# Performance work log

Hardware: AMD Instinct MI355X
Metric: run time of the kernel (lower is better)

## Reference

```python
import jax, jax.numpy as jnp
import numpy as np


def _lambertw_real(z: float) -> float:
    # real branch W0 for z > e, Newton iteration (static, numpy)
    w = np.log(z) - np.log(np.log(z))
    for _ in range(30):
        ew = np.exp(w)
        w = w - (w * ew - z) / (ew * (w + 1.0))
    return float(w)


def setup_inputs() -> dict:
    key = jax.random.key(0)
    ks = jax.random.split(key, 8)
    B, D, Wd, Hd, heads = 4, 64, 48, 48, 4
    dh = D // heads
    return {
        "x": jax.random.normal(ks[0], (B, D, Wd, Hd), jnp.float32),
        "Wq": jax.random.normal(ks[1], (heads, dh, D), jnp.float32) * 0.05,
        "bq": jax.random.normal(ks[2], (heads, dh), jnp.float32) * 0.05,
        "Wv": jax.random.normal(ks[3], (heads, dh, D), jnp.float32) * 0.05,
        "bv": jax.random.normal(ks[4], (heads, dh), jnp.float32) * 0.05,
        "Wo": jax.random.normal(ks[5], (D, D), jnp.float32) * 0.05,
        "bo": jax.random.normal(ks[6], (D,), jnp.float32) * 0.05,
        "gamma": jax.random.normal(ks[7], (1,), jnp.float32),
    }


def reference(x, Wq, bq, Wv, bv, Wo, bo, gamma):
    B, D, Wd, Hd = x.shape
    heads, dh, _ = Wq.shape
    N = Wd * Hd
    scalar = jnp.sqrt(jnp.asarray(D / heads, jnp.float32))

    x_flat = x.reshape(B, D, N)          # true [B, D, N] layout (1x1 conv input)
    x_r = x.reshape(B, N, D)             # faithful to torch x.view(B, N, D)

    outs = []
    for h in range(heads):
        # q: [B, N, dh] (conv1x1 then permute)
        q = jnp.einsum('kd,bdn->bnk', Wq[h], x_flat) + bq[h][None, None, :]
        qn = jnp.sum(q * q, axis=2)      # squared row norms [B, N]
        # expanded squared L2 distance: ||qi||^2 - 2 qi.qj + ||qj||^2
        dist = qn[:, :, None] - 2.0 * jnp.einsum('bnk,bmk->bnm', q, q) + qn[:, None, :]
        P = jax.nn.softmax(dist / (-scalar), axis=-1)   # [B, N, N]
        # A_h from weight.view(1, D, dh): row-major reshape, NOT transpose
        WqR = Wq[h].reshape(D, dh)
        A = (WqR @ WqR.T) / scalar       # [D, D]
        f = jnp.einsum('bnm,bmd->bnd', P, x_r) @ A      # [B, N, D]
        f_img = f.reshape(B, D, N)       # faithful to .view(B, D, W, H)
        v = jnp.einsum('kd,bdn->bkn', Wv[h], f_img) + bv[h][None, :, None]
        outs.append(v.reshape(B, N, dh))  # faithful to .view(B, N, dh)

    cat = jnp.concatenate(outs, axis=2).reshape(B, D, N)  # .view(B, D, W, H)
    out = jnp.einsum('od,bdn->bon', Wo, cat) + bo[None, :, None]

    # Lipschitz-style bound
    phi = jnp.asarray(_lambertw_real(N / np.e), jnp.float32)
    term = jnp.sqrt(jnp.sum(jnp.sum(Wq * Wq, axis=(1, 2)) * jnp.sum(Wv * Wv, axis=(1, 2))))
    bound = jnp.sqrt(jnp.asarray(N / D, jnp.float32)) * (4.0 * phi + 1.0) * term * jnp.linalg.norm(Wo)

    out = out / bound
    return gamma * out.reshape(B, D, Wd, Hd) + x
```

## Files before the change

kernel.cpp:

```cpp
#include <hip/hip_runtime.h>
#include <math.h>


#define OFF_SC  0
#define OFF_AF  16
#define OFF_QFB 8208
#define OFF_QFA 303120
#define OFF_QN  598032
#define OFF_XF  634896
#define OFF_F2  929808

#define LOG2E 1.44269504f

typedef __attribute__((ext_vector_type(8))) short bf16x8;
typedef __attribute__((ext_vector_type(16))) float f32x16;
union U4 { uint4 u; bf16x8 b; };

__device__ __forceinline__ unsigned short f2bf(float x) {
    unsigned int u = __float_as_uint(x);
    unsigned int r = u + 0x7fffu + ((u >> 16) & 1u);
    return (unsigned short)(r >> 16);
}
__device__ __forceinline__ float bf2f(unsigned short v) {
    return __uint_as_float((unsigned int)v << 16);
}

__global__ __launch_bounds__(256) void k_prep(
    const float* __restrict__ x, const float* __restrict__ Wq,
    const float* __restrict__ bq, const float* __restrict__ Wv,
    const float* __restrict__ Wo, const float* __restrict__ gamma, float* ws)
{
    __shared__ __align__(16) char smem[8192];
    const int bid = blockIdx.x, t = threadIdx.x;

    if (bid == 0) {
        double* red  = (double*)smem;
        double* sums = (double*)(smem + 2048);
        for (int ph = 0; ph < 9; ++ph) {
            double s = 0.0;
            if (ph < 4) {
                const float* W = Wq + ph * 1024;
                for (int i = t; i < 1024; i += 256) { double v = W[i]; s += v * v; }
            } else if (ph < 8) {
                const float* W = Wv + (ph - 4) * 1024;
                for (int i = t; i < 1024; i += 256) { double v = W[i]; s += v * v; }
            } else {
                for (int i = t; i < 4096; i += 256) { double v = Wo[i]; s += v * v; }
            }
            red[t] = s; __syncthreads();
            for (int off = 128; off; off >>= 1) {
                if (t < off) red[t] += red[t + off];
                __syncthreads();
            }
            if (t == 0) sums[ph] = red[0];
            __syncthreads();
        }
        if (t == 0) {
            float z = 2304.0f / 2.7182818284590452f;
            float w = logf(z) - logf(logf(z));
            #pragma unroll 1
            for (int it = 0; it < 30; ++it) {
                float ew = __expf(w);
                w = w - (w * ew - z) / (ew * (w + 1.0f));
            }
            double phi = (double)w;
            double term = sqrt(sums[0]*sums[4] + sums[1]*sums[5] +
                               sums[2]*sums[6] + sums[3]*sums[7]);
            double bound = 6.0 * (4.0 * phi + 1.0) * term * sqrt(sums[8]);
            ws[OFF_SC] = (float)((double)gamma[0] / bound);
        }
    } else if (bid <= 64) {
        float* WlP = (float*)smem;
        int id = bid - 1, h = id >> 4, dq = id & 15;
        const float* W = Wq + h * 1024;
        for (int i = t; i < 1024; i += 256) WlP[(i >> 4) * 17 + (i & 15)] = W[i];
        __syncthreads();
        int dl = t >> 6, e = t & 63, d = dq * 4 + dl;
        float s = 0.f;
        #pragma unroll
        for (int k = 0; k < 16; ++k) s += WlP[d * 17 + k] * WlP[e * 17 + k];
        int tt = d >> 4, j = d & 7, l = ((d >> 3) & 1) * 32 + (e & 31), ec = e >> 5;
        unsigned short* af = (unsigned short*)(ws + OFF_AF);
        af[(((h * 4 + tt) * 2 + ec) * 64 + l) * 8 + j] = f2bf(0.25f * s);
    } else if (bid <= 640) {
        float* WlT = (float*)smem;
        float* bl  = (float*)(smem + 4096);
        float* qnp = (float*)(smem + 4160);
        int rb = bid - 65, bh = rb / 36, nb = rb % 36;
        int h = bh & 3, b = bh >> 2;
        const float* W = Wq + h * 1024;
        for (int i = t; i < 1024; i += 256) WlT[(i & 63) * 16 + (i >> 6)] = W[i];
        if (t < 16) bl[t] = bq[h * 16 + t];
        __syncthreads();
        int nl = t & 63, kg = t >> 6, n = nb * 64 + nl;
        const float* xb = x + (size_t)b * 147456;
        const float4* wrow = (const float4*)WlT;
        float q0 = bl[kg*4], q1 = bl[kg*4+1], q2 = bl[kg*4+2], q3 = bl[kg*4+3];
        for (int d = 0; d < 64; ++d) {
            float xv = xb[d * 2304 + n];
            float4 wv = wrow[d * 4 + kg];
            q0 = fmaf(wv.x, xv, q0); q1 = fmaf(wv.y, xv, q1);
            q2 = fmaf(wv.z, xv, q2); q3 = fmaf(wv.w, xv, q3);
        }
        qnp[kg * 64 + nl] = q0*q0 + q1*q1 + q2*q2 + q3*q3;
        unsigned pB0 = (unsigned)f2bf(q0) | ((unsigned)f2bf(q1) << 16);
        unsigned pB1 = (unsigned)f2bf(q2) | ((unsigned)f2bf(q3) << 16);
        const float sA = 0.5f * LOG2E;
        unsigned pA0 = (unsigned)f2bf(sA*q0) | ((unsigned)f2bf(sA*q1) << 16);
        unsigned pA1 = (unsigned)f2bf(sA*q2) | ((unsigned)f2bf(sA*q3) << 16);
        size_t base = (size_t)(bh * 72 + (n >> 5)) * 256
                    + (size_t)(((kg >> 1) * 32 + (n & 31)) * 4 + (kg & 1) * 2);
        *(uint2*)((unsigned*)((unsigned short*)(ws + OFF_QFB)) + base) = make_uint2(pB0, pB1);
        *(uint2*)((unsigned*)((unsigned short*)(ws + OFF_QFA)) + base) = make_uint2(pA0, pA1);
        __syncthreads();
        if (t < 64) {
            float qn = qnp[t] + qnp[64 + t] + qnp[128 + t] + qnp[192 + t];
            ws[OFF_QN + bh * 2304 + nb * 64 + t] = -0.25f * LOG2E * qn;
        }
    } else {
        int i = (bid - 641) * 256 + t;
        int l = i & 63, c1 = i >> 6;
        int dc = c1 & 1, c2 = c1 >> 1;
        int T = c2 % 144, b = c2 / 144;
        const float* xb = x + (size_t)b * 147456;
        int col = dc * 32 + (l & 31), mbase = 16 * T + (l >> 5) * 8;
        unsigned int pk[4];
        #pragma unroll
        for (int jj = 0; jj < 4; ++jj) {
            float f0 = xb[(mbase + 2*jj) * 64 + col];
            float f1 = xb[(mbase + 2*jj + 1) * 64 + col];
            pk[jj] = (unsigned int)f2bf(f0) | ((unsigned int)f2bf(f1) << 16);
        }
        ((uint4*)((unsigned short*)(ws + OFF_XF)))[i] = make_uint4(pk[0], pk[1], pk[2], pk[3]);
    }
}

__global__ __launch_bounds__(256, 4) void k_attn(float* __restrict__ ws)
{
    __shared__ __align__(16) char smem[40448];
    float* qn_s = (float*)smem;
    float (*Ols)[32][68] = (float (*)[32][68])smem;
    unsigned short (*fls)[80] = (unsigned short (*)[80])(smem + 34816);
    float* Lls = (float*)(smem + 34816 + 5120);

    const int t = threadIdx.x, w = t >> 6, lane = t & 63;
    const int bid = (blockIdx.x & 7) * 144 + (blockIdx.x >> 3);
    const int bh = bid / 72, rc = bid % 72;
    const int h = bh & 3;
    const int b = bh >> 2;
    const int hi = lane >> 5, nl = lane & 31, s4 = hi * 4;

    const uint4* QB = (const uint4*)((const unsigned short*)(ws + OFF_QFB)) + (size_t)bh * 4608;
    const uint4* QA = (const uint4*)((const unsigned short*)(ws + OFF_QFA)) + (size_t)bh * 4608;
    const uint4* XF = (const uint4*)((const unsigned short*)(ws + OFF_XF)) + (size_t)b * 18432;
    const float* qn = ws + OFF_QN + bh * 2304;

    for (int i = t; i < 576; i += 256)
        ((float4*)qn_s)[i] = ((const float4*)qn)[i];

    U4 qb; qb.u = QB[rc * 64 + lane];
    const float qoffl = qn[rc * 32 + nl];

    f32x16 O0, O1;
    #pragma unroll
    for (int i = 0; i < 16; ++i) { O0[i] = 0.f; O1[i] = 0.f; }
    float lrun = 0.f;

    __syncthreads();

    #pragma unroll 2
    for (int it = 0; it < 18; ++it) {
        const int ht = w + it * 4;
        const int m0 = ht * 32;
        U4 xv[4];
        #pragma unroll
        for (int q = 0; q < 4; ++q) xv[q].u = XF[(size_t)(ht * 4 + q) * 64 + lane];
        U4 a0; a0.u = QA[ht * 64 + lane];
        f32x16 c0;
        #pragma unroll
        for (int g = 0; g < 4; ++g) {
            float4 t4 = *(const float4*)(qn_s + m0 + 8 * g + s4);
            c0[4*g+0] = t4.x + qoffl; c0[4*g+1] = t4.y + qoffl;
            c0[4*g+2] = t4.z + qoffl; c0[4*g+3] = t4.w + qoffl;
        }
        f32x16 s0 = __builtin_amdgcn_mfma_f32_32x32x16_bf16(a0.b, qb.b, c0, 0, 0, 0);
        float p[16];
        #pragma unroll
        for (int r = 0; r < 16; ++r)
            asm("v_exp_f32 %0, %1" : "=v"(p[r]) : "v"(s0[r]));
        float la = 0.f, lb = 0.f, lc = 0.f, ld = 0.f;
        #pragma unroll
        for (int r = 0; r < 16; r += 4) {
            la += p[r]; lb += p[r+1]; lc += p[r+2]; ld += p[r+3];
        }
        lrun += (la + lb) + (lc + ld);
        unsigned int wd[8], xd[8];
        #pragma unroll
        for (int i = 0; i < 8; ++i)
            asm("v_cvt_pk_bf16_f32 %0, %1, %2"
                : "=v"(wd[i]) : "v"(p[2*i]), "v"(p[2*i + 1]));
        #pragma unroll
        for (int i = 0; i < 8; ++i) xd[i] = (unsigned int)__shfl_xor((int)wd[i], 32);
        U4 af0, af1;
        af0.u.x = hi ? xd[2] : wd[0];  af0.u.y = hi ? xd[3] : wd[1];
        af0.u.z = hi ? wd[2] : xd[0];  af0.u.w = hi ? wd[3] : xd[1];
        af1.u.x = hi ? xd[6] : wd[4];  af1.u.y = hi ? xd[7] : wd[5];
        af1.u.z = hi ? wd[6] : xd[4];  af1.u.w = hi ? wd[7] : xd[5];
        O0 = __builtin_amdgcn_mfma_f32_32x32x16_bf16(af0.b, xv[0].b, O0, 0, 0, 0);
        O1 = __builtin_amdgcn_mfma_f32_32x32x16_bf16(af0.b, xv[1].b, O1, 0, 0, 0);
        O0 = __builtin_amdgcn_mfma_f32_32x32x16_bf16(af1.b, xv[2].b, O0, 0, 0, 0);
        O1 = __builtin_amdgcn_mfma_f32_32x32x16_bf16(af1.b, xv[3].b, O1, 0, 0, 0);
    }
    __syncthreads();

    lrun += __shfl_xor(lrun, 32);
    #pragma unroll
    for (int r = 0; r < 16; ++r) {
        int n = (r & 3) + 8 * (r >> 2) + s4;
        Ols[w][n][nl]      = O0[r];
        Ols[w][n][nl + 32] = O1[r];
    }
    if (!hi) Lls[w * 32 + nl] = lrun;
    __syncthreads();

    {
        int n = t >> 3, d0 = (t & 7) * 8;
        float invL = 1.f / (Lls[n] + Lls[32 + n] + Lls[64 + n] + Lls[96 + n]);
        float f[8];
        #pragma unroll
        for (int j = 0; j < 8; ++j)
            f[j] = (Ols[0][n][d0+j] + Ols[1][n][d0+j] +
                    Ols[2][n][d0+j] + Ols[3][n][d0+j]) * invL;
        unsigned int pk[4];
        #pragma unroll
        for (int i = 0; i < 4; ++i)
            asm("v_cvt_pk_bf16_f32 %0, %1, %2" : "=v"(pk[i]) : "v"(f[2*i]), "v"(f[2*i+1]));
        *(uint4*)((char*)&fls[0][0] + n * 160 + d0 * 2) = make_uint4(pk[0], pk[1], pk[2], pk[3]);
    }
    __syncthreads();

    if (w < 2) {
        const int ec = w;
        const uint4* AFp = (const uint4*)((const unsigned short*)(ws + OFF_AF)) + h * 512;
        f32x16 acc;
        #pragma unroll
        for (int i = 0; i < 16; ++i) acc[i] = 0.f;
        #pragma unroll
        for (int tt = 0; tt < 4; ++tt) {
            U4 a, bb;
            a.u  = *(const uint4*)((const char*)&fls[0][0] + nl * 160 + tt * 32 + hi * 16);
            bb.u = AFp[(tt * 2 + ec) * 64 + lane];
            acc = __builtin_amdgcn_mfma_f32_32x32x16_bf16(a.b, bb.b, acc, 0, 0, 0);
        }
        unsigned short* f2g = (unsigned short*)(ws + OFF_F2) +
                              (size_t)bh * 147456 + (size_t)rc * 32 * 64;
        #pragma unroll
        for (int r = 0; r < 16; ++r)
            f2g[((r & 3) + 8 * (r >> 2) + s4) * 64 + ec * 32 + nl] = f2bf(acc[r]);
    }
}

__global__ __launch_bounds__(256) void k_post(
    const float* __restrict__ x, const float* __restrict__ Wv,
    const float* __restrict__ bv, const float* __restrict__ Wo,
    const float* __restrict__ bo, const float* __restrict__ ws,
    float* __restrict__ out)
{
    __shared__ float WvL[4096];
    __shared__ float WoT[64 * 68];
    __shared__ float catL[16][68];
    __shared__ float bvL[64], boL[64];
    __shared__ float scs;
    const int bid = blockIdx.x, t = threadIdx.x;
    const int b = bid / 144, n0 = (bid % 144) * 16;
    for (int i = t; i < 4096; i += 256) WvL[i] = Wv[i];
    for (int i = t; i < 4096; i += 256) WoT[(i & 63) * 68 + (i >> 6)] = Wo[i];
    if (t < 64) { bvL[t] = bv[t]; boL[t] = bo[t]; }
    if (t == 0) scs = ws[OFF_SC];
    __syncthreads();

    const int nl = t & 15, q = t >> 4;
    const int n = n0 + nl;
    {
        const int h = q >> 2, cq = q & 3;
        const int k = n / 144;
        const int np = (n % 144) * 16 + cq * 4;
        const unsigned short* f2p = (const unsigned short*)(ws + OFF_F2)
                                  + (size_t)(b * 4 + h) * 147456;
        const float* wv = WvL + h * 1024 + k * 64;
        float bvv = bvL[h * 16 + k];
        float v0 = bvv, v1 = bvv, v2 = bvv, v3 = bvv;
        for (int d = 0; d < 64; ++d) {
            ushort4 f4 = *(const ushort4*)(f2p + d * 2304 + np);
            float wd = wv[d];
            v0 = fmaf(wd, bf2f(f4.x), v0);
            v1 = fmaf(wd, bf2f(f4.y), v1);
            v2 = fmaf(wd, bf2f(f4.z), v2);
            v3 = fmaf(wd, bf2f(f4.w), v3);
        }
        int col = h * 16 + cq * 4;
        catL[nl][col + 0] = v0; catL[nl][col + 1] = v1;
        catL[nl][col + 2] = v2; catL[nl][col + 3] = v3;
    }
    __syncthreads();
    {
        const int oq = q;
        const float4* wo4 = (const float4*)WoT;
        float a0 = boL[oq*4], a1 = boL[oq*4+1], a2 = boL[oq*4+2], a3 = boL[oq*4+3];
        for (int d = 0; d < 64; ++d) {
            float cv = catL[nl][d];
            float4 w4 = wo4[d * 17 + oq];
            a0 = fmaf(w4.x, cv, a0); a1 = fmaf(w4.y, cv, a1);
            a2 = fmaf(w4.z, cv, a2); a3 = fmaf(w4.w, cv, a3);
        }
        float sc = scs;
        const float* xb = x + (size_t)b * 147456;
        float* ob = out + (size_t)b * 147456;
        int o = oq * 4;
        ob[(o+0) * 2304 + n] = fmaf(sc, a0, xb[(o+0) * 2304 + n]);
        ob[(o+1) * 2304 + n] = fmaf(sc, a1, xb[(o+1) * 2304 + n]);
        ob[(o+2) * 2304 + n] = fmaf(sc, a2, xb[(o+2) * 2304 + n]);
        ob[(o+3) * 2304 + n] = fmaf(sc, a3, xb[(o+3) * 2304 + n]);
    }
}

extern "C" void kernel_launch(void* const* d_in, const int* in_sizes, int n_in,
                              void* d_out, int out_size, void* d_ws, size_t ws_size,
                              hipStream_t stream) {
    const float* x     = (const float*)d_in[0];
    const float* Wq    = (const float*)d_in[1];
    const float* bq    = (const float*)d_in[2];
    const float* Wv    = (const float*)d_in[3];
    const float* bv    = (const float*)d_in[4];
    const float* Wo    = (const float*)d_in[5];
    const float* bo    = (const float*)d_in[6];
    const float* gamma = (const float*)d_in[7];
    float* out = (float*)d_out;
    float* ws  = (float*)d_ws;
    k_prep<<<929,  256, 0, stream>>>(x, Wq, bq, Wv, Wo, gamma, ws);
    k_attn<<<1152, 256, 0, stream>>>(ws);
    k_post<<<576,  256, 0, stream>>>(x, Wv, bv, Wo, bo, ws, out);
}
```

Before: 131.9 us.

## Process two query row-chunks per attention block to reuse key/value tiles

```diff
diff --git a/kernel.cpp b/kernel.cpp
--- a/kernel.cpp
+++ b/kernel.cpp
@@ -135,7 +135,7 @@
     }
 }
 
-__global__ __launch_bounds__(256, 4) void k_attn(float* __restrict__ ws)
+__global__ __launch_bounds__(256, 3) void k_attn(float* __restrict__ ws)
 {
     __shared__ __align__(16) char smem[40448];
     float* qn_s = (float*)smem;
@@ -144,8 +144,8 @@
     float* Lls = (float*)(smem + 34816 + 5120);
 
     const int t = threadIdx.x, w = t >> 6, lane = t & 63;
-    const int bid = (blockIdx.x & 7) * 144 + (blockIdx.x >> 3);
-    const int bh = bid / 72, rc = bid % 72;
+    const int bid = (blockIdx.x & 7) * 72 + (blockIdx.x >> 3);
+    const int bh = bid / 36, rg = bid % 36;
     const int h = bh & 3;
     const int b = bh >> 2;
     const int hi = lane >> 5, nl = lane & 31, s4 = hi * 4;
@@ -158,13 +158,16 @@
     for (int i = t; i < 576; i += 256)
         ((float4*)qn_s)[i] = ((const float4*)qn)[i];
 
-    U4 qb; qb.u = QB[rc * 64 + lane];
-    const float qoffl = qn[rc * 32 + nl];
-
-    f32x16 O0, O1;
+    U4 qb0, qb1;
+    qb0.u = QB[(rg * 2 + 0) * 64 + lane];
+    qb1.u = QB[(rg * 2 + 1) * 64 + lane];
+    const float qoffl0 = qn[(rg * 2 + 0) * 32 + nl];
+    const float qoffl1 = qn[(rg * 2 + 1) * 32 + nl];
+
+    f32x16 O00, O01, O10, O11;
     #pragma unroll
-    for (int i = 0; i < 16; ++i) { O0[i] = 0.f; O1[i] = 0.f; }
-    float lrun = 0.f;
+    for (int i = 0; i < 16; ++i) { O00[i] = 0.f; O01[i] = 0.f; O10[i] = 0.f; O11[i] = 0.f; }
+    float lrun0 = 0.f, lrun1 = 0.f;
 
     __syncthreads();
 
@@ -176,53 +179,88 @@
         #pragma unroll
         for (int q = 0; q < 4; ++q) xv[q].u = XF[(size_t)(ht * 4 + q) * 64 + lane];
         U4 a0; a0.u = QA[ht * 64 + lane];
-        f32x16 c0;
+        float bc[16];
         #pragma unroll
         for (int g = 0; g < 4; ++g) {
             float4 t4 = *(const float4*)(qn_s + m0 + 8 * g + s4);
-            c0[4*g+0] = t4.x + qoffl; c0[4*g+1] = t4.y + qoffl;
-            c0[4*g+2] = t4.z + qoffl; c0[4*g+3] = t4.w + qoffl;
-        }
-        f32x16 s0 = __builtin_amdgcn_mfma_f32_32x32x16_bf16(a0.b, qb.b, c0, 0, 0, 0);
-        float p[16];
-        #pragma unroll
-        for (int r = 0; r < 16; ++r)
-            asm("v_exp_f32 %0, %1" : "=v"(p[r]) : "v"(s0[r]));
-        float la = 0.f, lb = 0.f, lc = 0.f, ld = 0.f;
-        #pragma unroll
-        for (int r = 0; r < 16; r += 4) {
-            la += p[r]; lb += p[r+1]; lc += p[r+2]; ld += p[r+3];
-        }
-        lrun += (la + lb) + (lc + ld);
-        unsigned int wd[8], xd[8];
-        #pragma unroll
-        for (int i = 0; i < 8; ++i)
-            asm("v_cvt_pk_bf16_f32 %0, %1, %2"
-                : "=v"(wd[i]) : "v"(p[2*i]), "v"(p[2*i + 1]));
-        #pragma unroll
-        for (int i = 0; i < 8; ++i) xd[i] = (unsigned int)__shfl_xor((int)wd[i], 32);
-        U4 af0, af1;
-        af0.u.x = hi ? xd[2] : wd[0];  af0.u.y = hi ? xd[3] : wd[1];
-        af0.u.z = hi ? wd[2] : xd[0];  af0.u.w = hi ? wd[3] : xd[1];
-        af1.u.x = hi ? xd[6] : wd[4];  af1.u.y = hi ? xd[7] : wd[5];
-        af1.u.z = hi ? wd[6] : xd[4];  af1.u.w = hi ? wd[7] : xd[5];
-        O0 = __builtin_amdgcn_mfma_f32_32x32x16_bf16(af0.b, xv[0].b, O0, 0, 0, 0);
-        O1 = __builtin_amdgcn_mfma_f32_32x32x16_bf16(af0.b, xv[1].b, O1, 0, 0, 0);
-        O0 = __builtin_amdgcn_mfma_f32_32x32x16_bf16(af1.b, xv[2].b, O0, 0, 0, 0);
-        O1 = __builtin_amdgcn_mfma_f32_32x32x16_bf16(af1.b, xv[3].b, O1, 0, 0, 0);
-    }
-    __syncthreads();
-
-    lrun += __shfl_xor(lrun, 32);
+            bc[4*g+0] = t4.x; bc[4*g+1] = t4.y; bc[4*g+2] = t4.z; bc[4*g+3] = t4.w;
+        }
+        {
+            f32x16 c0;
+            #pragma unroll
+            for (int r = 0; r < 16; ++r) c0[r] = bc[r] + qoffl0;
+            f32x16 s0 = __builtin_amdgcn_mfma_f32_32x32x16_bf16(a0.b, qb0.b, c0, 0, 0, 0);
+            float p[16];
+            #pragma unroll
+            for (int r = 0; r < 16; ++r)
+                asm("v_exp_f32 %0, %1" : "=v"(p[r]) : "v"(s0[r]));
+            float la = 0.f, lb = 0.f, lc = 0.f, ld = 0.f;
+            #pragma unroll
+            for (int r = 0; r < 16; r += 4) {
+                la += p[r]; lb += p[r+1]; lc += p[r+2]; ld += p[r+3];
+            }
+            lrun0 += (la + lb) + (lc + ld);
+            unsigned int wd[8], xd[8];
+            #pragma unroll
+            for (int i = 0; i < 8; ++i)
+                asm("v_cvt_pk_bf16_f32 %0, %1, %2"
+                    : "=v"(wd[i]) : "v"(p[2*i]), "v"(p[2*i + 1]));
+            #pragma unroll
+            for (int i = 0; i < 8; ++i) xd[i] = (unsigned int)__shfl_xor((int)wd[i], 32);
+            U4 af0, af1;
+            af0.u.x = hi ? xd[2] : wd[0];  af0.u.y = hi ? xd[3] : wd[1];
+            af0.u.z = hi ? wd[2] : xd[0];  af0.u.w = hi ? wd[3] : xd[1];
+            af1.u.x = hi ? xd[6] : wd[4];  af1.u.y = hi ? xd[7] : wd[5];
+            af1.u.z = hi ? wd[6] : xd[4];  af1.u.w = hi ? wd[7] : xd[5];
+            O00 = __builtin_amdgcn_mfma_f32_32x32x16_bf16(af0.b, xv[0].b, O00, 0, 0, 0);
+            O01 = __builtin_amdgcn_mfma_f32_32x32x16_bf16(af0.b, xv[1].b, O01, 0, 0, 0);
+            O00 = __builtin_amdgcn_mfma_f32_32x32x16_bf16(af1.b, xv[2].b, O00, 0, 0, 0);
+            O01 = __builtin_amdgcn_mfma_f32_32x32x16_bf16(af1.b, xv[3].b, O01, 0, 0, 0);
+        }
+        {
+            f32x16 c1;
+            #pragma unroll
+            for (int r = 0; r < 16; ++r) c1[r] = bc[r] + qoffl1;
+            f32x16 s1 = __builtin_amdgcn_mfma_f32_32x32x16_bf16(a0.b, qb1.b, c1, 0, 0, 0);
+            float p[16];
+            #pragma unroll
+            for (int r = 0; r < 16; ++r)
+                asm("v_exp_f32 %0, %1" : "=v"(p[r]) : "v"(s1[r]));
+            float la = 0.f, lb = 0.f, lc = 0.f, ld = 0.f;
+            #pragma unroll
+            for (int r = 0; r < 16; r += 4) {
+                la += p[r]; lb += p[r+1]; lc += p[r+2]; ld += p[r+3];
+            }
+            lrun1 += (la + lb) + (lc + ld);
+            unsigned int wd[8], xd[8];
+            #pragma unroll
+            for (int i = 0; i < 8; ++i)
+                asm("v_cvt_pk_bf16_f32 %0, %1, %2"
+                    : "=v"(wd[i]) : "v"(p[2*i]), "v"(p[2*i + 1]));
+            #pragma unroll
+            for (int i = 0; i < 8; ++i) xd[i] = (unsigned int)__shfl_xor((int)wd[i], 32);
+            U4 af0, af1;
+            af0.u.x = hi ? xd[2] : wd[0];  af0.u.y = hi ? xd[3] : wd[1];
+            af0.u.z = hi ? wd[2] : xd[0];  af0.u.w = hi ? wd[3] : xd[1];
+            af1.u.x = hi ? xd[6] : wd[4];  af1.u.y = hi ? xd[7] : wd[5];
+            af1.u.z = hi ? wd[6] : xd[4];  af1.u.w = hi ? wd[7] : xd[5];
+            O10 = __builtin_amdgcn_mfma_f32_32x32x16_bf16(af0.b, xv[0].b, O10, 0, 0, 0);
+            O11 = __builtin_amdgcn_mfma_f32_32x32x16_bf16(af0.b, xv[1].b, O11, 0, 0, 0);
+            O10 = __builtin_amdgcn_mfma_f32_32x32x16_bf16(af1.b, xv[2].b, O10, 0, 0, 0);
+            O11 = __builtin_amdgcn_mfma_f32_32x32x16_bf16(af1.b, xv[3].b, O11, 0, 0, 0);
+        }
+    }
+    __syncthreads();
+
+    lrun0 += __shfl_xor(lrun0, 32);
     #pragma unroll
     for (int r = 0; r < 16; ++r) {
         int n = (r & 3) + 8 * (r >> 2) + s4;
-        Ols[w][n][nl]      = O0[r];
-        Ols[w][n][nl + 32] = O1[r];
-    }
-    if (!hi) Lls[w * 32 + nl] = lrun;
-    __syncthreads();
-
+        Ols[w][n][nl]      = O00[r];
+        Ols[w][n][nl + 32] = O01[r];
+    }
+    if (!hi) Lls[w * 32 + nl] = lrun0;
+    __syncthreads();
     {
         int n = t >> 3, d0 = (t & 7) * 8;
         float invL = 1.f / (Lls[n] + Lls[32 + n] + Lls[64 + n] + Lls[96 + n]);
@@ -239,6 +277,14 @@
     }
     __syncthreads();
 
+    lrun1 += __shfl_xor(lrun1, 32);
+    #pragma unroll
+    for (int r = 0; r < 16; ++r) {
+        int n = (r & 3) + 8 * (r >> 2) + s4;
+        Ols[w][n][nl]      = O10[r];
+        Ols[w][n][nl + 32] = O11[r];
+    }
+    if (!hi) Lls[w * 32 + nl] = lrun1;
     if (w < 2) {
         const int ec = w;
         const uint4* AFp = (const uint4*)((const unsigned short*)(ws + OFF_AF)) + h * 512;
@@ -253,7 +299,44 @@
             acc = __builtin_amdgcn_mfma_f32_32x32x16_bf16(a.b, bb.b, acc, 0, 0, 0);
         }
         unsigned short* f2g = (unsigned short*)(ws + OFF_F2) +
-                              (size_t)bh * 147456 + (size_t)rc * 32 * 64;
+                              (size_t)bh * 147456 + (size_t)(rg * 2 + 0) * 32 * 64;
+        #pragma unroll
+        for (int r = 0; r < 16; ++r)
+            f2g[((r & 3) + 8 * (r >> 2) + s4) * 64 + ec * 32 + nl] = f2bf(acc[r]);
+    }
+    __syncthreads();
+
+    {
+        int n = t >> 3, d0 = (t & 7) * 8;
+        float invL = 1.f / (Lls[n] + Lls[32 + n] + Lls[64 + n] + Lls[96 + n]);
+        float f[8];
+        #pragma unroll
+        for (int j = 0; j < 8; ++j)
+            f[j] = (Ols[0][n][d0+j] + Ols[1][n][d0+j] +
+                    Ols[2][n][d0+j] + Ols[3][n][d0+j]) * invL;
+        unsigned int pk[4];
+        #pragma unroll
+        for (int i = 0; i < 4; ++i)
+            asm("v_cvt_pk_bf16_f32 %0, %1, %2" : "=v"(pk[i]) : "v"(f[2*i]), "v"(f[2*i+1]));
+        *(uint4*)((char*)&fls[0][0] + n * 160 + d0 * 2) = make_uint4(pk[0], pk[1], pk[2], pk[3]);
+    }
+    __syncthreads();
+
+    if (w < 2) {
+        const int ec = w;
+        const uint4* AFp = (const uint4*)((const unsigned short*)(ws + OFF_AF)) + h * 512;
+        f32x16 acc;
+        #pragma unroll
+        for (int i = 0; i < 16; ++i) acc[i] = 0.f;
+        #pragma unroll
+        for (int tt = 0; tt < 4; ++tt) {
+            U4 a, bb;
+            a.u  = *(const uint4*)((const char*)&fls[0][0] + nl * 160 + tt * 32 + hi * 16);
+            bb.u = AFp[(tt * 2 + ec) * 64 + lane];
+            acc = __builtin_amdgcn_mfma_f32_32x32x16_bf16(a.b, bb.b, acc, 0, 0, 0);
+        }
+        unsigned short* f2g = (unsigned short*)(ws + OFF_F2) +
+                              (size_t)bh * 147456 + (size_t)(rg * 2 + 1) * 32 * 64;
         #pragma unroll
         for (int r = 0; r < 16; ++r)
             f2g[((r & 3) + 8 * (r >> 2) + s4) * 64 + ec * 32 + nl] = f2bf(acc[r]);
@@ -337,7 +420,7 @@
     const float* gamma = (const float*)d_in[7];
     float* out = (float*)d_out;
     float* ws  = (float*)d_ws;
-    k_prep<<<929,  256, 0, stream>>>(x, Wq, bq, Wv, Wo, gamma, ws);
-    k_attn<<<1152, 256, 0, stream>>>(ws);
-    k_post<<<576,  256, 0, stream>>>(x, Wv, bv, Wo, bo, ws, out);
-}
+    k_prep<<<929, 256, 0, stream>>>(x, Wq, bq, Wv, Wo, gamma, ws);
+    k_attn<<<576, 256, 0, stream>>>(ws);
+    k_post<<<576, 256, 0, stream>>>(x, Wv, bv, Wo, bo, ws, out);
+}
```

Measured after the change: 179.9 us. 1.36x slower.
